# Kernel tuning notes

Hardware: AMD Instinct MI355X
Metric: run time of the kernel (lower is better)

Reference implementation:

```python
import jax, jax.numpy as jnp
import numpy as np

TIME_WEIGHT = 0.1
CURRENT_TIME = 0.0

def setup_inputs() -> dict:
    key = jax.random.key(0)
    k1, k2, k3, k4, k5 = jax.random.split(key, 5)
    B, M, D, C = 131072, 100, 1024, 16
    return {
        "query": jax.random.normal(k1, (B, D), dtype=jnp.float32),
        "context": jax.random.normal(k2, (B, C), dtype=jnp.float32),
        "mem_keys": jax.random.normal(k3, (M, D), dtype=jnp.float32),
        "mem_values": jax.random.normal(k4, (M, D), dtype=jnp.float32),
        "mem_contexts": jax.random.normal(k5, (M, C), dtype=jnp.float32),
        "mem_timestamps": jnp.zeros((M, 1), dtype=jnp.float32),
    }

def reference(query, context, mem_keys, mem_values, mem_contexts, mem_timestamps):
    # content scores: [B, M]
    scores = jnp.einsum('bd,md->bm', query, mem_keys)
    # contextual binding
    scores = scores + 0.5 * jnp.einsum('bc,mc->bm', context, mem_contexts)
    # exponential time-decay bias, broadcast over batch: [M]
    time_decay = jnp.exp(-TIME_WEIGHT * (CURRENT_TIME - mem_timestamps.squeeze(-1)))
    scores = scores + time_decay[None, :]
    attn = jax.nn.softmax(scores, axis=-1)
    return jnp.einsum('bm,md->bd', attn, mem_values)
```

## Files before the change

### kernel.cpp

```cpp
#include <hip/hip_runtime.h>


typedef __attribute__((ext_vector_type(8))) _Float16 f16x8;
typedef __attribute__((ext_vector_type(4))) float f32x4;

constexpr int DQ = 1024, CD = 16, MM = 100, KD = 1056, NT = 7;
constexpr size_t KE = (size_t)112 * KD;

constexpr int QBUF = 16384, KOFF = 49152, KBUF = 7168;
constexpr int VOFF = 32768, VBUF = 8192;
constexpr int LDSZ = 70656;

#define WAITV(n) asm volatile("s_waitcnt vmcnt(" #n ")" ::: "memory")

__device__ __forceinline__ void gl16(const void* g, void* l) {
    __builtin_amdgcn_global_load_lds(
        (const __attribute__((address_space(1))) unsigned int*)g,
        (__attribute__((address_space(3))) unsigned int*)l, 16, 0, 0);
}

__global__ void build_k(const float* __restrict__ mk, const float* __restrict__ mc,
                        _Float16* __restrict__ KH)
{
    int d = blockIdx.x * 64 + threadIdx.x;
    int m = blockIdx.y;
    if (d >= KD) return;
    float x = 0.f;
    if (m < MM) {
        if (d < DQ)            x = mk[(size_t)m * DQ + d];
        else if (d < DQ + CD)  x = 0.5f * mc[(size_t)m * CD + (d - DQ)];
    }
    KH[(size_t)m * KD + d] = (_Float16)x;
}

__global__ void build_vt(const float* __restrict__ mv, _Float16* __restrict__ VT)
{
    int idx = blockIdx.x * 256 + threadIdx.x;
    int d = idx >> 7, m = idx & 127;
    VT[idx] = (m < MM) ? (_Float16)mv[(size_t)m * DQ + d] : (_Float16)0.f;
}

__global__ __launch_bounds__(512, 4)
void epmem_pipe(const float* __restrict__ q, const float* __restrict__ cx,
                const float* __restrict__ ts,
                const _Float16* __restrict__ KH, const _Float16* __restrict__ VT,
                float* __restrict__ out)
{
    __shared__ __align__(16) char lds[LDSZ];

    const int t = threadIdx.x, w = t >> 6, lane = t & 63;
    const int lr = lane & 15, lk = lane >> 4;
    const int row0 = blockIdx.x * 128;

    float dec[NT];
    #pragma unroll
    for (int nt = 0; nt < NT; ++nt) {
        int m = nt * 16 + lr;
        dec[nt] = (m < MM) ? __expf(0.1f * ts[m]) : 0.f;
    }

    auto stageQ = [&](int buf, int ks) {
        char* dst = lds + buf * QBUF;
        #pragma unroll
        for (int i = 0; i < 2; ++i) {
            int s = i * 512 + w * 64 + lane;
            int row = s >> 3;
            int logical = (s & 7) ^ (row & 7);
            gl16(q + (size_t)(row0 + row) * DQ + ks * 32 + logical * 4,
                 dst + (i * 512 + w * 64) * 16);
        }
    };
    auto stageQctx = [&](int buf) {
        char* dst = lds + buf * QBUF;
        gl16(cx + (size_t)(row0 + (t >> 2)) * CD + (t & 3) * 4, dst + (w * 64) * 16);
    };
    auto stageK = [&](int buf, int ks) {
        if (w < 7) {
            char* dst = lds + KOFF + buf * KBUF;
            int s = w * 64 + lane;
            int m = s >> 2;
            int logical = (s & 3) ^ ((m >> 1) & 3);
            gl16(KH + (size_t)m * KD + ks * 32 + logical * 8, dst + (w * 64) * 16);
        }
    };
    auto stageV = [&](int buf, int c) {
        char* dst = lds + VOFF + buf * VBUF;
        int d = t >> 4;
        int logical = (t & 15) ^ (d & 15);
        gl16(VT + (size_t)(c * 32 + d) * 128 + logical * 8, dst + (w * 64) * 16);
    };

    f32x4 acc[NT];
    #pragma unroll
    for (int nt = 0; nt < NT; ++nt) acc[nt] = (f32x4){0.f, 0.f, 0.f, 0.f};

    stageQ(0, 0); stageK(0, 0);
    stageQ(1, 1); stageK(1, 1);
    if (w < 7) { WAITV(3); } else { WAITV(2); }
    __builtin_amdgcn_s_barrier();

    int bc = 0;
    for (int ks = 0; ks <= 32; ++ks) {
        int bs = bc + 2; if (bs >= 3) bs -= 3;
        if (ks + 2 < 32)       { stageQ(bs, ks + 2); stageK(bs, ks + 2); }
        else if (ks + 2 == 32) { stageQctx(bs);      stageK(bs, 32); }

        const char* qb = lds + bc * QBUF;
        f16x8 ah, al;
        if (ks < 32) {
            const char* base = qb + (w * 16 + lr) * 128;
            const int g = lr & 7;
            f32x4 x = *(const f32x4*)(base + (((2 * lk)     ^ g) << 4));
            f32x4 y = *(const f32x4*)(base + (((2 * lk + 1) ^ g) << 4));
            #pragma unroll
            for (int e = 0; e < 4; ++e) {
                _Float16 h = (_Float16)x[e]; ah[e] = h;     al[e] = (_Float16)(x[e] - (float)h);
                h = (_Float16)y[e];          ah[4 + e] = h; al[4 + e] = (_Float16)(y[e] - (float)h);
            }
        } else {
            if (lk < 2) {
                const char* base = qb + (w * 16 + lr) * 64;
                f32x4 x = *(const f32x4*)(base + (2 * lk) * 16);
                f32x4 y = *(const f32x4*)(base + (2 * lk + 1) * 16);
                #pragma unroll
                for (int e = 0; e < 4; ++e) {
                    _Float16 h = (_Float16)x[e]; ah[e] = h;     al[e] = (_Float16)(x[e] - (float)h);
                    h = (_Float16)y[e];          ah[4 + e] = h; al[4 + e] = (_Float16)(y[e] - (float)h);
                }
            } else {
                #pragma unroll
                for (int e = 0; e < 8; ++e) { ah[e] = (_Float16)0.f; al[e] = (_Float16)0.f; }
            }
        }
        #pragma unroll
        for (int nt = 0; nt < NT; ++nt) {
            int m = nt * 16 + lr;
            f16x8 bh = *(const f16x8*)(lds + KOFF + bc * KBUF
                         + ((m << 2) + (lk ^ ((lr >> 1) & 3))) * 16);
            acc[nt] = __builtin_amdgcn_mfma_f32_16x16x32_f16(ah, bh, acc[nt], 0, 0, 0);
            acc[nt] = __builtin_amdgcn_mfma_f32_16x16x32_f16(al, bh, acc[nt], 0, 0, 0);
        }
        if (ks <= 29)      { if (w < 7) { WAITV(3); } else { WAITV(2); } }
        else if (ks == 30) { if (w < 7) { WAITV(2); } else { WAITV(1); } }
        else if (ks == 31) { WAITV(0); }
        if (ks < 32) __builtin_amdgcn_s_barrier();
        if (++bc == 3) bc = 0;
    }

    __builtin_amdgcn_s_barrier();
    stageV(0, 0); stageV(1, 1);

    char* Pb = lds + w * 4096;
    {
        float rm[4] = {-3e38f, -3e38f, -3e38f, -3e38f};
        #pragma unroll
        for (int nt = 0; nt < NT; ++nt) {
            int m = nt * 16 + lr;
            #pragma unroll
            for (int r = 0; r < 4; ++r) {
                float s = (m < MM) ? (acc[nt][r] + dec[nt]) : -3e38f;
                acc[nt][r] = s;
                rm[r] = fmaxf(rm[r], s);
            }
        }
        #pragma unroll
        for (int r = 0; r < 4; ++r)
            #pragma unroll
            for (int off = 1; off < 16; off <<= 1)
                rm[r] = fmaxf(rm[r], __shfl_xor(rm[r], off));
        float rs[4] = {0.f, 0.f, 0.f, 0.f};
        #pragma unroll
        for (int nt = 0; nt < NT; ++nt)
            #pragma unroll
            for (int r = 0; r < 4; ++r) {
                float e = __expf(acc[nt][r] - rm[r]);
                acc[nt][r] = e;
                rs[r] += e;
            }
        #pragma unroll
        for (int r = 0; r < 4; ++r)
            #pragma unroll
            for (int off = 1; off < 16; off <<= 1)
                rs[r] += __shfl_xor(rs[r], off);
        #pragma unroll
        for (int r = 0; r < 4; ++r) {
            float inv = 1.f / rs[r];
            int row = 4 * lk + r;
            #pragma unroll
            for (int nt = 0; nt < NT; ++nt)
                *(_Float16*)(Pb + row * 256 + (((nt * 2 + (lr >> 3)) ^ row) & 15) * 16
                             + (lr & 7) * 2) = (_Float16)(acc[nt][r] * inv);
        }
    }
    if (lane < 32) {
        int row = lane >> 1, sl = 14 + (lane & 1);
        uint4 z = {0u, 0u, 0u, 0u};
        *(uint4*)(Pb + row * 256 + ((sl ^ row) & 15) * 16) = z;
    }
    WAITV(1);
    __builtin_amdgcn_s_barrier();

    f16x8 pa[4];
    #pragma unroll
    for (int k4 = 0; k4 < 4; ++k4)
        pa[k4] = *(const f16x8*)(Pb + lr * 256 + (((k4 * 4 + lk) ^ lr) & 15) * 16);

    int vc = 0;
    for (int c = 0; c < 32; ++c) {
        int vs = vc + 2; if (vs >= 3) vs -= 3;
        if (c + 2 < 32) stageV(vs, c + 2);
        f32x4 o0 = {0.f, 0.f, 0.f, 0.f}, o1 = {0.f, 0.f, 0.f, 0.f};
        #pragma unroll
        for (int k4 = 0; k4 < 4; ++k4) {
            const char* vb = lds + VOFF + vc * VBUF + (((k4 * 4 + lk) ^ lr) & 15) * 16;
            f16x8 b0 = *(const f16x8*)(vb + lr * 256);
            f16x8 b1 = *(const f16x8*)(vb + (16 + lr) * 256);
            o0 = __builtin_amdgcn_mfma_f32_16x16x32_f16(pa[k4], b0, o0, 0, 0, 0);
            o1 = __builtin_amdgcn_mfma_f32_16x16x32_f16(pa[k4], b1, o1, 0, 0, 0);
        }
        #pragma unroll
        for (int r = 0; r < 4; ++r) {
            size_t rw = (size_t)(row0 + w * 16 + 4 * lk + r) * DQ + c * 32;
            __builtin_nontemporal_store(o0[r], &out[rw + lr]);
            __builtin_nontemporal_store(o1[r], &out[rw + 16 + lr]);
        }
        if (c == 0)       { WAITV(9); }
        else if (c <= 29) { WAITV(17); }
        else if (c == 30) { WAITV(16); }
        if (c < 31) __builtin_amdgcn_s_barrier();
        if (++vc == 3) vc = 0;
    }
}

extern "C" void kernel_launch(void* const* d_in, const int* in_sizes, int n_in,
                              void* d_out, int out_size, void* d_ws, size_t ws_size,
                              hipStream_t stream) {
    const float* q  = (const float*)d_in[0];
    const float* cx = (const float*)d_in[1];
    const float* mk = (const float*)d_in[2];
    const float* mv = (const float*)d_in[3];
    const float* mc = (const float*)d_in[4];
    const float* ts = (const float*)d_in[5];
    float* out = (float*)d_out;

    _Float16* wsp = (_Float16*)d_ws;
    _Float16* KH = wsp;
    _Float16* VT = wsp + KE;

    const int B = in_sizes[0] / DQ;

    build_k<<<dim3(17, 112), dim3(64), 0, stream>>>(mk, mc, KH);
    build_vt<<<dim3(512), dim3(256), 0, stream>>>(mv, VT);
    epmem_pipe<<<dim3(B / 128), dim3(512), 0, stream>>>(q, cx, ts, KH, VT, out);
}
```

Measured before the change: 296.3 us.

## Load query directly into registers instead of staging through LDS

Query fp32 tiles are no longer copied into LDS with global_load_lds and swizzled. Each lane now loads its own MFMA operand fragment straight from global memory into registers with nontemporal loads, double-buffered two k-steps ahead. Only K and the context tile stay staged in LDS. This is meant to cut LDS traffic and shrink the LDS footprint, which could raise occupancy. The cost is more VGPR pressure, less-coalesced 32-byte-per-lane global reads, and a reworked vmcnt wait schedule that must match the new counts.

```diff
diff --git a/kernel.cpp b/kernel.cpp
--- a/kernel.cpp
+++ b/kernel.cpp
@@ -7,9 +7,9 @@
 constexpr int DQ = 1024, CD = 16, MM = 100, KD = 1056, NT = 7;
 constexpr size_t KE = (size_t)112 * KD;
 
-constexpr int QBUF = 16384, KOFF = 49152, KBUF = 7168;
+constexpr int KOFF = 8192, KBUF = 7168;
 constexpr int VOFF = 32768, VBUF = 8192;
-constexpr int LDSZ = 70656;
+constexpr int LDSZ = 57344;
 
 #define WAITV(n) asm volatile("s_waitcnt vmcnt(" #n ")" ::: "memory")
 
@@ -59,20 +59,8 @@
         dec[nt] = (m < MM) ? __expf(0.1f * ts[m]) : 0.f;
     }
 
-    auto stageQ = [&](int buf, int ks) {
-        char* dst = lds + buf * QBUF;
-        #pragma unroll
-        for (int i = 0; i < 2; ++i) {
-            int s = i * 512 + w * 64 + lane;
-            int row = s >> 3;
-            int logical = (s & 7) ^ (row & 7);
-            gl16(q + (size_t)(row0 + row) * DQ + ks * 32 + logical * 4,
-                 dst + (i * 512 + w * 64) * 16);
-        }
-    };
-    auto stageQctx = [&](int buf) {
-        char* dst = lds + buf * QBUF;
-        gl16(cx + (size_t)(row0 + (t >> 2)) * CD + (t & 3) * 4, dst + (w * 64) * 16);
+    auto stageCtx = [&]() {
+        gl16(cx + (size_t)(row0 + (t >> 2)) * CD + (t & 3) * 4, lds + (w * 64) * 16);
     };
     auto stageK = [&](int buf, int ks) {
         if (w < 7) {
@@ -94,60 +82,86 @@
     #pragma unroll
     for (int nt = 0; nt < NT; ++nt) acc[nt] = (f32x4){0.f, 0.f, 0.f, 0.f};
 
-    stageQ(0, 0); stageK(0, 0);
-    stageQ(1, 1); stageK(1, 1);
-    if (w < 7) { WAITV(3); } else { WAITV(2); }
+    const float* qp = q + (size_t)(row0 + w * 16 + lr) * DQ + 8 * lk;
+
+    auto qkStep = [&](f32x4 x, f32x4 y, int ks) {
+        f16x8 ah, al;
+        #pragma unroll
+        for (int e = 0; e < 4; ++e) {
+            _Float16 h = (_Float16)x[e]; ah[e] = h;     al[e] = (_Float16)(x[e] - (float)h);
+            h = (_Float16)y[e];          ah[4 + e] = h; al[4 + e] = (_Float16)(y[e] - (float)h);
+        }
+        const char* kb = lds + KOFF + (ks % 3) * KBUF;
+        #pragma unroll
+        for (int nt = 0; nt < NT; ++nt) {
+            int m = nt * 16 + lr;
+            f16x8 bh = *(const f16x8*)(kb + ((m << 2) + (lk ^ ((lr >> 1) & 3))) * 16);
+            acc[nt] = __builtin_amdgcn_mfma_f32_16x16x32_f16(ah, bh, acc[nt], 0, 0, 0);
+            acc[nt] = __builtin_amdgcn_mfma_f32_16x16x32_f16(al, bh, acc[nt], 0, 0, 0);
+        }
+    };
+
+    stageCtx();
+    stageK(0, 0); stageK(1, 1);
+    f32x4 qA0 = __builtin_nontemporal_load((const f32x4*)(qp + 0));
+    f32x4 qA1 = __builtin_nontemporal_load((const f32x4*)(qp + 4));
+    f32x4 qB0 = __builtin_nontemporal_load((const f32x4*)(qp + 32));
+    f32x4 qB1 = __builtin_nontemporal_load((const f32x4*)(qp + 36));
+    WAITV(0);
     __builtin_amdgcn_s_barrier();
 
-    int bc = 0;
-    for (int ks = 0; ks <= 32; ++ks) {
-        int bs = bc + 2; if (bs >= 3) bs -= 3;
-        if (ks + 2 < 32)       { stageQ(bs, ks + 2); stageK(bs, ks + 2); }
-        else if (ks + 2 == 32) { stageQctx(bs);      stageK(bs, 32); }
-
-        const char* qb = lds + bc * QBUF;
+    for (int ks = 0; ks < 32; ks += 2) {
+        stageK((ks + 2) % 3, ks + 2);
+        f32x4 nx0, nx1;
+        if (ks <= 28) {
+            nx0 = __builtin_nontemporal_load((const f32x4*)(qp + (ks + 2) * 32));
+            nx1 = __builtin_nontemporal_load((const f32x4*)(qp + (ks + 2) * 32 + 4));
+        }
+        qkStep(qA0, qA1, ks);
+        if (ks <= 28) { qA0 = nx0; qA1 = nx1; }
+        if (ks <= 28) { if (w < 7) { WAITV(3); } else { WAITV(2); } }
+        else          { if (w < 7) { WAITV(1); } else { WAITV(0); } }
+        __builtin_amdgcn_s_barrier();
+
+        if (ks <= 28) stageK((ks + 3) % 3, ks + 3);
+        f32x4 ny0, ny1;
+        if (ks <= 28) {
+            ny0 = __builtin_nontemporal_load((const f32x4*)(qp + (ks + 3) * 32));
+            ny1 = __builtin_nontemporal_load((const f32x4*)(qp + (ks + 3) * 32 + 4));
+        }
+        qkStep(qB0, qB1, ks + 1);
+        if (ks <= 28) { qB0 = ny0; qB1 = ny1; }
+        if (ks <= 28) { if (w < 7) { WAITV(3); } else { WAITV(2); } }
+        else          { WAITV(0); }
+        __builtin_amdgcn_s_barrier();
+    }
+
+    {
         f16x8 ah, al;
-        if (ks < 32) {
-            const char* base = qb + (w * 16 + lr) * 128;
-            const int g = lr & 7;
-            f32x4 x = *(const f32x4*)(base + (((2 * lk)     ^ g) << 4));
-            f32x4 y = *(const f32x4*)(base + (((2 * lk + 1) ^ g) << 4));
+        if (lk < 2) {
+            const char* base = lds + (w * 16 + lr) * 64;
+            f32x4 x = *(const f32x4*)(base + (2 * lk) * 16);
+            f32x4 y = *(const f32x4*)(base + (2 * lk + 1) * 16);
             #pragma unroll
             for (int e = 0; e < 4; ++e) {
                 _Float16 h = (_Float16)x[e]; ah[e] = h;     al[e] = (_Float16)(x[e] - (float)h);
                 h = (_Float16)y[e];          ah[4 + e] = h; al[4 + e] = (_Float16)(y[e] - (float)h);
             }
         } else {
-            if (lk < 2) {
-                const char* base = qb + (w * 16 + lr) * 64;
-                f32x4 x = *(const f32x4*)(base + (2 * lk) * 16);
-                f32x4 y = *(const f32x4*)(base + (2 * lk + 1) * 16);
-                #pragma unroll
-                for (int e = 0; e < 4; ++e) {
-                    _Float16 h = (_Float16)x[e]; ah[e] = h;     al[e] = (_Float16)(x[e] - (float)h);
-                    h = (_Float16)y[e];          ah[4 + e] = h; al[4 + e] = (_Float16)(y[e] - (float)h);
-                }
-            } else {
-                #pragma unroll
-                for (int e = 0; e < 8; ++e) { ah[e] = (_Float16)0.f; al[e] = (_Float16)0.f; }
-            }
-        }
+            #pragma unroll
+            for (int e = 0; e < 8; ++e) { ah[e] = (_Float16)0.f; al[e] = (_Float16)0.f; }
+        }
+        const char* kb = lds + KOFF + 2 * KBUF;
         #pragma unroll
         for (int nt = 0; nt < NT; ++nt) {
             int m = nt * 16 + lr;
-            f16x8 bh = *(const f16x8*)(lds + KOFF + bc * KBUF
-                         + ((m << 2) + (lk ^ ((lr >> 1) & 3))) * 16);
+            f16x8 bh = *(const f16x8*)(kb + ((m << 2) + (lk ^ ((lr >> 1) & 3))) * 16);
             acc[nt] = __builtin_amdgcn_mfma_f32_16x16x32_f16(ah, bh, acc[nt], 0, 0, 0);
             acc[nt] = __builtin_amdgcn_mfma_f32_16x16x32_f16(al, bh, acc[nt], 0, 0, 0);
         }
-        if (ks <= 29)      { if (w < 7) { WAITV(3); } else { WAITV(2); } }
-        else if (ks == 30) { if (w < 7) { WAITV(2); } else { WAITV(1); } }
-        else if (ks == 31) { WAITV(0); }
-        if (ks < 32) __builtin_amdgcn_s_barrier();
-        if (++bc == 3) bc = 0;
-    }
-
-    __builtin_amdgcn_s_barrier();
+    }
+    __syncthreads();
+
     stageV(0, 0); stageV(1, 1);
 
     char* Pb = lds + w * 4096;
```

New measurement: 317.7 us. +7.3%, slower.
